# Kernel tuning notes

Hardware: AMD Instinct MI355X
Metric: run time of the kernel (lower is better)

The kernel has to match this reference:

```python
import jax, jax.numpy as jnp
import numpy as np

N_NODES = 50000
N_EDGES = 800000
D_IN = 128
D_H = 128
N_LAYERS = 3
N_CLASSES = 10
NUM_GRAPHS = 256
BN_EPS = 1e-5


def _bn(h, gamma, beta):
    # BatchNorm1d, training-mode statistics (biased variance) over node axis
    mu = jnp.mean(h, axis=0)
    var = jnp.mean((h - mu) ** 2, axis=0)
    return (h - mu) * jax.lax.rsqrt(var + BN_EPS) * gamma + beta


def setup_inputs() -> dict:
    key = jax.random.key(0)
    ks = jax.random.split(key, 16)
    x = jax.random.normal(ks[0], (N_NODES, D_IN), dtype=jnp.float32)
    edge_index = jax.random.randint(ks[1], (2, N_EDGES), 0, N_NODES, dtype=jnp.int64)
    batch = jnp.sort(jax.random.randint(ks[2], (N_NODES,), 0, NUM_GRAPHS, dtype=jnp.int64))
    s1 = 1.0 / np.sqrt(D_IN)
    s2 = 1.0 / np.sqrt(D_H)
    W1 = jax.random.uniform(ks[3], (N_LAYERS, D_IN, D_H), jnp.float32, -s1, s1)
    b1 = jax.random.uniform(ks[4], (N_LAYERS, D_H), jnp.float32, -s1, s1)
    g1 = jnp.ones((N_LAYERS, D_H), jnp.float32)
    bt1 = jnp.zeros((N_LAYERS, D_H), jnp.float32)
    W2 = jax.random.uniform(ks[5], (N_LAYERS, D_H, D_H), jnp.float32, -s2, s2)
    b2 = jax.random.uniform(ks[6], (N_LAYERS, D_H), jnp.float32, -s2, s2)
    g2 = jnp.ones((N_LAYERS, D_H), jnp.float32)
    bt2 = jnp.zeros((N_LAYERS, D_H), jnp.float32)
    sc = 1.0 / np.sqrt(D_H * N_LAYERS)
    Wc1 = jax.random.uniform(ks[7], (D_H * N_LAYERS, D_H), jnp.float32, -sc, sc)
    bc1 = jax.random.uniform(ks[8], (D_H,), jnp.float32, -sc, sc)
    Wc2 = jax.random.uniform(ks[9], (D_H, N_CLASSES), jnp.float32, -s2, s2)
    bc2 = jax.random.uniform(ks[10], (N_CLASSES,), jnp.float32, -s2, s2)
    return {"x": x, "edge_index": edge_index, "batch": batch,
            "W1": W1, "b1": b1, "g1": g1, "bt1": bt1,
            "W2": W2, "b2": b2, "g2": g2, "bt2": bt2,
            "Wc1": Wc1, "bc1": bc1, "Wc2": Wc2, "bc2": bc2}


def reference(x, edge_index, batch, W1, b1, g1, bt1, W2, b2, g2, bt2, Wc1, bc1, Wc2, bc2):
    src = edge_index[0]
    dst = edge_index[1]
    readouts = []
    h = x
    for i in range(N_LAYERS):
        # GINConv, eps=0: (1+eps)*h + sum_{j->i} h_j, then MLP
        agg = jax.ops.segment_sum(h[src], dst, num_segments=N_NODES)  # [N, d]
        z = h + agg
        z = z @ W1[i] + b1[i]
        z = jax.nn.relu(_bn(z, g1[i], bt1[i]))
        z = z @ W2[i] + b2[i]
        # outer BN + ReLU
        h = jax.nn.relu(_bn(z, g2[i], bt2[i]))
        readouts.append(jax.ops.segment_sum(h, batch, num_segments=NUM_GRAPHS))
    h_graph = jnp.concatenate(readouts, axis=1)  # [G, L*d]
    # classifier (dropout in eval mode -> identity)
    out = jax.nn.relu(h_graph @ Wc1 + bc1) @ Wc2 + bc2
    return out
```

## Files before the change

### kernel.cpp

```cpp
#include <hip/hip_runtime.h>

#define N_NODES 50000
#define N_EDGES 800000
#define D 128
#define NLAYERS 3
#define N_CLASSES 10
#define NUM_GRAPHS 256
#define BN_EPS 1e-5f

#define CHUNKS 64
#define CHSIZE 12500
#define RANGES 4
#define RSIZE 12500
#define SBANKS 8

typedef __attribute__((ext_vector_type(4))) float f4;
typedef __attribute__((ext_vector_type(2))) float f2;
typedef __attribute__((ext_vector_type(4))) int i4;
typedef __attribute__((ext_vector_type(8))) short short8;
typedef __attribute__((ext_vector_type(4))) unsigned short us4;
typedef __attribute__((ext_vector_type(8))) unsigned short us8;

__device__ inline float b2f(unsigned short u) {
    unsigned int i = ((unsigned int)u) << 16;
    return __builtin_bit_cast(float, i);
}
__device__ inline unsigned short f2b(float f) {
    unsigned int u = __builtin_bit_cast(unsigned int, f);
    unsigned int r = (u + 0x7FFFu + ((u >> 16) & 1u)) >> 16;
    return (unsigned short)r;
}

__device__ inline void coef_to_lds(const float* __restrict__ stats,
                                   const float* __restrict__ g,
                                   const float* __restrict__ bt,
                                   float* ac_sm, int tid) {
    if (tid < D) {
        float s = 0.f, q = 0.f;
#pragma unroll
        for (int b = 0; b < SBANKS; b++) {
            s += stats[b * 2 * D + tid];
            q += stats[b * 2 * D + D + tid];
        }
        float mu = s * (1.0f / N_NODES);
        float var = q * (1.0f / N_NODES) - mu * mu;
        float inv = rsqrtf(var + BN_EPS);
        float a = g[tid] * inv;
        ac_sm[tid] = a;
        ac_sm[D + tid] = bt[tid] - mu * a;
    }
}


__global__ __launch_bounds__(256) void k_ph(const int* __restrict__ dst,
                                            int* __restrict__ pos,
                                            int* __restrict__ ph) {
    __shared__ int h[RSIZE];
    int c = blockIdx.x, r = blockIdx.y;
    int t = threadIdx.x;
    for (int i = t; i < RSIZE; i += 256) h[i] = 0;
    __syncthreads();
    int base = c * CHSIZE;
    int lo = r * RSIZE;
    const i4* dst4 = (const i4*)(dst + base);
    for (int j = t; j < CHSIZE / 4; j += 256) {
        i4 dv = dst4[j];
#pragma unroll
        for (int u = 0; u < 4; u++) {
            int d = dv[u] - lo;
            if ((unsigned)d < RSIZE) pos[base + j * 4 + u] = atomicAdd(&h[d], 1);
        }
    }
    __syncthreads();
    int* outp = ph + (size_t)c * N_NODES + lo;
    for (int i = t; i < RSIZE; i += 256) outp[i] = h[i];
}

__global__ __launch_bounds__(256) void k_m1(int* __restrict__ ph,
                                            const int* __restrict__ bat,
                                            int* __restrict__ deg,
                                            int* __restrict__ bsum,
                                            int* __restrict__ gp) {
    __shared__ int sm[256];
    int t = threadIdx.x;
    int b = blockIdx.x * 256 + t;
    int s = 0;
    if (b < N_NODES) {
#pragma unroll 4
        for (int c = 0; c < CHUNKS; c++) {
            int v = ph[(size_t)c * N_NODES + b];
            ph[(size_t)c * N_NODES + b] = s;
            s += v;
        }
        deg[b] = s;
    }
    sm[t] = s;
    __syncthreads();
    for (int off = 128; off > 0; off >>= 1) {
        if (t < off) sm[t] += sm[t + off];
        __syncthreads();
    }
    if (t == 0) bsum[blockIdx.x] = sm[0];
    if (b < N_NODES) {
        int bb = bat[b];
        int prev = (b == 0) ? -1 : bat[b - 1];
        for (int g = prev + 1; g <= bb; g++) gp[g] = b;
        if (b == N_NODES - 1)
            for (int g = bb + 1; g <= NUM_GRAPHS; g++) gp[g] = N_NODES;
    }
}


__global__ __launch_bounds__(256) void k_xw(const float* __restrict__ x,
                                            const float* __restrict__ W1,
                                            const float* __restrict__ W2,
                                            us4* __restrict__ xb,
                                            short8* __restrict__ Wb) {
    int gid = blockIdx.x * 256 + threadIdx.x;
    const f4* xf = (const f4*)x;
#pragma unroll
    for (int rep = 0; rep < 2; rep++) {
        int i = gid + rep * 800000;
        f4 v = xf[i];
        us4 o;
        o[0] = f2b(v.x); o[1] = f2b(v.y); o[2] = f2b(v.z); o[3] = f2b(v.w);
        xb[i] = o;
    }
    if (gid < 6 * 32 * 64) {
        int m = gid >> 11;
        int f = (gid >> 6) & 31;
        int l = gid & 63;
        int ct = f >> 2, ks = f & 3;
        int n = ct * 16 + (l & 15);
        int k0 = ks * 32 + (l >> 4) * 8;
        const float* Wsrc = (m < 3) ? (W1 + (size_t)m * D * D) : (W2 + (size_t)(m - 3) * D * D);
        short8 o;
#pragma unroll
        for (int j = 0; j < 8; j++) o[j] = (short)f2b(Wsrc[(size_t)(k0 + j) * D + n]);
        Wb[gid] = o;
    }
}


__global__ void k_s2(int* __restrict__ bsum, int* __restrict__ rowp) {
    __shared__ int sm[256];
    int t = threadIdx.x;
    int v = (t < 196) ? bsum[t] : 0;
    sm[t] = v;
    __syncthreads();
    for (int off = 1; off < 256; off <<= 1) {
        int u = (t >= off) ? sm[t - off] : 0;
        __syncthreads();
        sm[t] += u;
        __syncthreads();
    }
    if (t < 196) bsum[t] = sm[t] - v;
    if (t == 195) rowp[N_NODES] = sm[t];
}

__global__ void k_s3(const int* __restrict__ deg, const int* __restrict__ bsum,
                     int* __restrict__ rowp) {
    __shared__ int sm[256];
    int t = threadIdx.x;
    int i = blockIdx.x * 256 + t;
    int v = (i < N_NODES) ? deg[i] : 0;
    sm[t] = v;
    __syncthreads();
    for (int off = 1; off < 256; off <<= 1) {
        int u = (t >= off) ? sm[t - off] : 0;
        __syncthreads();
        sm[t] += u;
        __syncthreads();
    }
    if (i < N_NODES) rowp[i] = bsum[blockIdx.x] + sm[t] - v;
}

__global__ __launch_bounds__(256) void k_scatter(const int* __restrict__ src,
                                                 const int* __restrict__ dst,
                                                 const int* __restrict__ pos,
                                                 const int* __restrict__ ph,
                                                 const int* __restrict__ rowp,
                                                 int* __restrict__ csr) {
    int e0 = (blockIdx.x * 256 + threadIdx.x) * 4;
    if (e0 >= N_EDGES) return;
    i4 sv = *(const i4*)(src + e0);
    i4 dv = *(const i4*)(dst + e0);
    i4 pv = *(const i4*)(pos + e0);
#pragma unroll
    for (int u = 0; u < 4; u++) {
        int cc = (e0 + u) / CHSIZE;
        int d = dv[u];
        csr[rowp[d] + ph[(size_t)cc * N_NODES + d] + pv[u]] = sv[u];
    }
}


template <bool APPLY_T>
__global__ __launch_bounds__(256) void k_agg(const us8* __restrict__ H,
                                             const float* __restrict__ stats,
                                             const float* __restrict__ g,
                                             const float* __restrict__ bt,
                                             const int* __restrict__ rowp,
                                             const int* __restrict__ csr,
                                             us8* __restrict__ U) {
    __shared__ float ac_sm[2 * D];
    int tid = threadIdx.x;
    if (APPLY_T) {
        coef_to_lds(stats, g, bt, ac_sm, tid);
        __syncthreads();
    }
    int gid = blockIdx.x * 256 + tid;
    int node = gid >> 4;
    int lane = tid & 15;
    float av[8], cv[8];
    if (APPLY_T) {
#pragma unroll
        for (int i = 0; i < 8; i++) {
            av[i] = ac_sm[lane * 8 + i];
            cv[i] = ac_sm[D + lane * 8 + i];
        }
    }
    float s[8] = {0.f, 0.f, 0.f, 0.f, 0.f, 0.f, 0.f, 0.f};
    auto accum = [&](us8 v) {
#pragma unroll
        for (int i = 0; i < 8; i++) {
            float f = b2f(v[i]);
            if (APPLY_T) f = fmaxf(f * av[i] + cv[i], 0.f);
            s[i] += f;
        }
    };
    accum(H[(size_t)node * 16 + lane]);
    int beg = rowp[node], end = rowp[node + 1];
    int j = beg;
    for (; j + 8 <= end; j += 8) {
        int idx[8];
#pragma unroll
        for (int u = 0; u < 8; u++) idx[u] = csr[j + u];
        us8 v[8];
#pragma unroll
        for (int u = 0; u < 8; u++) v[u] = H[(size_t)idx[u] * 16 + lane];
#pragma unroll
        for (int u = 0; u < 8; u++) accum(v[u]);
    }
    for (; j + 2 <= end; j += 2) {
        int i0 = csr[j], i1 = csr[j + 1];
        us8 v0 = H[(size_t)i0 * 16 + lane];
        us8 v1 = H[(size_t)i1 * 16 + lane];
        accum(v0); accum(v1);
    }
    if (j < end) accum(H[(size_t)csr[j] * 16 + lane]);
    us8 o;
#pragma unroll
    for (int i = 0; i < 8; i++) o[i] = f2b(s[i]);
    U[(size_t)node * 16 + lane] = o;
}


template <bool TRANS>
__global__ __launch_bounds__(256) void k_gemm(const unsigned short* __restrict__ A,
                                              const short8* __restrict__ Wb,
                                              const float* __restrict__ bias,
                                              const float* __restrict__ stats_in,
                                              const float* __restrict__ g,
                                              const float* __restrict__ bt,
                                              unsigned short* __restrict__ Z,
                                              float* __restrict__ stats_out, int M) {
    __shared__ float lds_s[D], lds_q[D];
    __shared__ float ac_sm[2 * D];
    int tid = threadIdx.x;
    if (tid < D) { lds_s[tid] = 0.f; lds_q[tid] = 0.f; }
    if (TRANS) coef_to_lds(stats_in, g, bt, ac_sm, tid);
    int w = tid >> 6, l = tid & 63;
    int lr = l & 15, lg = l >> 4;
    int rowb0 = blockIdx.x * 128 + w * 32;
    f4 acc[2][8];
#pragma unroll
    for (int ct = 0; ct < 8; ct++) {
        float bv = bias[ct * 16 + lr];
#pragma unroll
        for (int rt = 0; rt < 2; rt++) {
            acc[rt][ct].x = bv; acc[rt][ct].y = bv; acc[rt][ct].z = bv; acc[rt][ct].w = bv;
        }
    }
    __syncthreads();

#pragma unroll
    for (int ks = 0; ks < 4; ks++) {
        short8 a[2];
#pragma unroll
        for (int rt = 0; rt < 2; rt++) {
            int arow = rowb0 + rt * 16 + lr;
            int arow_c = arow < M ? arow : M - 1;
            if (!TRANS) {
                a[rt] = *(const short8*)(A + (size_t)arow_c * D + ks * 32 + lg * 8);
            } else {
                int k0 = ks * 32 + lg * 8;
                const unsigned short* ap = A + (size_t)arow_c * D + k0;
                us4 v0 = *(const us4*)ap;
                us4 v1 = *(const us4*)(ap + 4);
                f4 a0 = *(const f4*)&ac_sm[k0];
                f4 a1 = *(const f4*)&ac_sm[k0 + 4];
                f4 c0 = *(const f4*)&ac_sm[D + k0];
                f4 c1 = *(const f4*)&ac_sm[D + k0 + 4];
                a[rt][0] = (short)f2b(fmaxf(b2f(v0[0]) * a0.x + c0.x, 0.f));
                a[rt][1] = (short)f2b(fmaxf(b2f(v0[1]) * a0.y + c0.y, 0.f));
                a[rt][2] = (short)f2b(fmaxf(b2f(v0[2]) * a0.z + c0.z, 0.f));
                a[rt][3] = (short)f2b(fmaxf(b2f(v0[3]) * a0.w + c0.w, 0.f));
                a[rt][4] = (short)f2b(fmaxf(b2f(v1[0]) * a1.x + c1.x, 0.f));
                a[rt][5] = (short)f2b(fmaxf(b2f(v1[1]) * a1.y + c1.y, 0.f));
                a[rt][6] = (short)f2b(fmaxf(b2f(v1[2]) * a1.z + c1.z, 0.f));
                a[rt][7] = (short)f2b(fmaxf(b2f(v1[3]) * a1.w + c1.w, 0.f));
            }
        }
#pragma unroll
        for (int ct = 0; ct < 8; ct++) {
            short8 b = Wb[(ct * 4 + ks) * 64 + l];
            acc[0][ct] = __builtin_amdgcn_mfma_f32_16x16x32_bf16(a[0], b, acc[0][ct], 0, 0, 0);
            acc[1][ct] = __builtin_amdgcn_mfma_f32_16x16x32_bf16(a[1], b, acc[1][ct], 0, 0, 0);
        }
    }

#pragma unroll
    for (int ct = 0; ct < 8; ct++) {
        float s = 0.f, q = 0.f;
#pragma unroll
        for (int rt = 0; rt < 2; rt++) {
#pragma unroll
            for (int r = 0; r < 4; r++) {
                float v = acc[rt][ct][r];
                int rd = rowb0 + rt * 16 + lg * 4 + r;
                float m = rd < M ? 1.f : 0.f;
                s += v * m;
                q += v * v * m;
                if (rd < M) Z[(size_t)rd * D + ct * 16 + lr] = f2b(v);
            }
        }
        s += __shfl_xor(s, 16);
        s += __shfl_xor(s, 32);
        q += __shfl_xor(q, 16);
        q += __shfl_xor(q, 32);
        if (lg == 0) {
            atomicAdd(&lds_s[ct * 16 + lr], s);
            atomicAdd(&lds_q[ct * 16 + lr], q);
        }
    }
    __syncthreads();
    int bank = blockIdx.x & (SBANKS - 1);
    if (tid < D) {
        atomicAdd(&stats_out[bank * 2 * D + tid], lds_s[tid]);
        atomicAdd(&stats_out[bank * 2 * D + D + tid], lds_q[tid]);
    }
}


__global__ __launch_bounds__(256) void k_readout(const unsigned int* __restrict__ Zb,
                                                 const float* __restrict__ stats,
                                                 const float* __restrict__ g,
                                                 const float* __restrict__ bt,
                                                 const int* __restrict__ gp,
                                                 const int* __restrict__ batch,
                                                 float* __restrict__ ro, int layer) {
    __shared__ f2 sm[256];
    __shared__ float ac_sm[2 * D];
    int tid = threadIdx.x;
    coef_to_lds(stats, g, bt, ac_sm, tid);
    __syncthreads();
    int n0 = blockIdx.x * 256;
    int n1 = n0 + 256; if (n1 > N_NODES) n1 = N_NODES;
    int g_lo = batch[n0], g_hi = batch[n1 - 1];
    int grp = tid >> 6, cw = tid & 63;
    float a0 = ac_sm[2 * cw], a1 = ac_sm[2 * cw + 1];
    float c0 = ac_sm[D + 2 * cw], c1 = ac_sm[D + 2 * cw + 1];
    for (int gg = g_lo; gg <= g_hi; gg++) {
        int beg = gp[gg]; if (beg < n0) beg = n0;
        int end = gp[gg + 1]; if (end > n1) end = n1;
        f2 acc; acc.x = 0.f; acc.y = 0.f;
        for (int r = beg + grp; r < end; r += 4) {
            unsigned int v = Zb[(size_t)r * 64 + cw];
            float x0 = b2f((unsigned short)(v & 0xFFFFu));
            float x1 = b2f((unsigned short)(v >> 16));
            acc.x += fmaxf(x0 * a0 + c0, 0.f);
            acc.y += fmaxf(x1 * a1 + c1, 0.f);
        }
        sm[tid] = acc;
        __syncthreads();
        if (tid < 64) {
            f2 t = sm[tid];
            t.x += sm[tid + 64].x + sm[tid + 128].x + sm[tid + 192].x;
            t.y += sm[tid + 64].y + sm[tid + 128].y + sm[tid + 192].y;
            atomicAdd(&ro[(size_t)gg * (NLAYERS * D) + layer * D + 2 * cw], t.x);
            atomicAdd(&ro[(size_t)gg * (NLAYERS * D) + layer * D + 2 * cw + 1], t.y);
        }
        __syncthreads();
    }
}


__global__ void k_cls(const float* __restrict__ ro, const float* __restrict__ Wc1,
                      const float* __restrict__ bc1, const float* __restrict__ Wc2,
                      const float* __restrict__ bc2, float* __restrict__ out) {
    __shared__ float r_sm[NLAYERS * D];
    __shared__ float h_sm[D];
    int g = blockIdx.x;
    int t = threadIdx.x;
    for (int i = t; i < NLAYERS * D; i += D) r_sm[i] = ro[(size_t)g * (NLAYERS * D) + i];
    __syncthreads();
    float acc = bc1[t];
    for (int k = 0; k < NLAYERS * D; k++) acc += r_sm[k] * Wc1[(size_t)k * D + t];
    h_sm[t] = fmaxf(acc, 0.f);
    __syncthreads();
    if (t < N_CLASSES) {
        float o = bc2[t];
        for (int k = 0; k < D; k++) o += h_sm[k] * Wc2[k * N_CLASSES + t];
        out[g * N_CLASSES + t] = o;
    }
}


extern "C" void kernel_launch(void* const* d_in, const int* in_sizes, int n_in,
                              void* d_out, int out_size, void* d_ws, size_t ws_size,
                              hipStream_t stream) {
    const float* x   = (const float*)d_in[0];
    const int*   ei  = (const int*)d_in[1];
    const int*   bat = (const int*)d_in[2];
    const float* W1  = (const float*)d_in[3];
    const float* b1  = (const float*)d_in[4];
    const float* g1  = (const float*)d_in[5];
    const float* bt1 = (const float*)d_in[6];
    const float* W2  = (const float*)d_in[7];
    const float* b2  = (const float*)d_in[8];
    const float* g2  = (const float*)d_in[9];
    const float* bt2 = (const float*)d_in[10];
    const float* Wc1 = (const float*)d_in[11];
    const float* bc1 = (const float*)d_in[12];
    const float* Wc2 = (const float*)d_in[13];
    const float* bc2 = (const float*)d_in[14];
    float* out = (float*)d_out;

    const int* src = ei;
    const int* dst = ei + N_EDGES;

    char* ws = (char*)d_ws;
    size_t off = 0;
    auto alloc = [&](size_t bytes) -> void* {
        void* p = ws + off;
        off += (bytes + 255) & ~(size_t)255;
        return p;
    };
    float* stats = (float*)alloc(6 * SBANKS * 2 * D * sizeof(float));
    float* ro    = (float*)alloc((size_t)NUM_GRAPHS * NLAYERS * D * sizeof(float));
    size_t zero_bytes = off;
    int*   deg   = (int*)alloc(N_NODES * sizeof(int));
    int*   gp    = (int*)alloc((NUM_GRAPHS + 1) * sizeof(int));
    int*   bsum  = (int*)alloc(256 * sizeof(int));
    int*   rowp  = (int*)alloc((N_NODES + 1) * sizeof(int));
    int*   pos   = (int*)alloc(N_EDGES * sizeof(int));
    int*   csr   = (int*)alloc(N_EDGES * sizeof(int));
    const size_t NBH = (size_t)N_NODES * D * sizeof(unsigned short);
    unsigned short* xb   = (unsigned short*)alloc(NBH);
    unsigned short* bufA = (unsigned short*)alloc(NBH);
    unsigned short* bufB = (unsigned short*)alloc(NBH);
    unsigned short* bufC = (unsigned short*)alloc(NBH);
    short8* Wb   = (short8*)alloc(6 * 32 * 64 * sizeof(short8));
    int* ph = (int*)bufB;

    hipMemsetAsync(ws, 0, zero_bytes, stream);

    k_ph<<<dim3(CHUNKS, RANGES), 256, 0, stream>>>(dst, pos, ph);
    k_m1<<<196, 256, 0, stream>>>(ph, bat, deg, bsum, gp);
    k_xw<<<3125, 256, 0, stream>>>(x, W1, W2, (us4*)xb, Wb);
    k_s2<<<1, 256, 0, stream>>>(bsum, rowp);
    k_s3<<<196, 256, 0, stream>>>(deg, bsum, rowp);
    k_scatter<<<(N_EDGES / 4 + 255) / 256, 256, 0, stream>>>(src, dst, pos, ph, rowp, csr);

    const int gemm_grid = (N_NODES + 127) / 128;
    const unsigned short* H = xb;
    for (int i = 0; i < NLAYERS; i++) {
        float* st1 = stats + (size_t)(2 * i) * SBANKS * 2 * D;
        float* st2 = stats + (size_t)(2 * i + 1) * SBANKS * 2 * D;
        float* st2p = stats + (size_t)(2 * i - 1) * SBANKS * 2 * D;
        if (i == 0)
            k_agg<false><<<3125, 256, 0, stream>>>((const us8*)H, nullptr, nullptr, nullptr,
                                                   rowp, csr, (us8*)bufA);
        else
            k_agg<true><<<3125, 256, 0, stream>>>((const us8*)H, st2p, g2 + (i - 1) * D,
                                                  bt2 + (i - 1) * D, rowp, csr, (us8*)bufA);
        k_gemm<false><<<gemm_grid, 256, 0, stream>>>(bufA, Wb + (size_t)i * 2048, b1 + i * D,
                                                     nullptr, nullptr, nullptr, bufB, st1, N_NODES);
        k_gemm<true><<<gemm_grid, 256, 0, stream>>>(bufB, Wb + (size_t)(3 + i) * 2048, b2 + i * D,
                                                    st1, g1 + i * D, bt1 + i * D, bufC, st2, N_NODES);
        k_readout<<<196, 256, 0, stream>>>((const unsigned int*)bufC, st2, g2 + i * D, bt2 + i * D,
                                           gp, bat, ro, i);
        H = bufC;
    }
    k_cls<<<NUM_GRAPHS, 128, 0, stream>>>(ro, Wc1, bc1, Wc2, bc2, out);
}
```

Baseline: 346.7 us.

## Slice feature buffers into 16-column planes, sort nodes by degree, use 16-bit indices

Node feature buffers are stored as 8 feature slices of 16 columns each. Each aggregation block now works on one slice, so the gathered working set per pass is smaller and more cache friendly. Nodes are also reordered by degree through a histogram and permutation, so threads within a wave see similar neighbour counts, which cuts divergence. CSR indices and positions become 16-bit to halve index traffic. The 16-bit node ids and positions rely on node ids fitting in unsigned short, but N_NODES is 50000, which fits.

```diff
diff --git a/kernel.cpp b/kernel.cpp
--- a/kernel.cpp
+++ b/kernel.cpp
@@ -13,6 +13,8 @@
 #define RANGES 4
 #define RSIZE 12500
 #define SBANKS 8
+#define NBLK 196
+#define SLICE 800000
 
 typedef __attribute__((ext_vector_type(4))) float f4;
 typedef __attribute__((ext_vector_type(2))) float f2;
@@ -31,6 +33,7 @@
     return (unsigned short)r;
 }
 
+
 __device__ inline void coef_to_lds(const float* __restrict__ stats,
                                    const float* __restrict__ g,
                                    const float* __restrict__ bt,
@@ -53,7 +56,7 @@
 
 
 __global__ __launch_bounds__(256) void k_ph(const int* __restrict__ dst,
-                                            int* __restrict__ pos,
+                                            unsigned short* __restrict__ pos,
                                             int* __restrict__ ph) {
     __shared__ int h[RSIZE];
     int c = blockIdx.x, r = blockIdx.y;
@@ -68,7 +71,7 @@
 #pragma unroll
         for (int u = 0; u < 4; u++) {
             int d = dv[u] - lo;
-            if ((unsigned)d < RSIZE) pos[base + j * 4 + u] = atomicAdd(&h[d], 1);
+            if ((unsigned)d < RSIZE) pos[base + j * 4 + u] = (unsigned short)atomicAdd(&h[d], 1);
         }
     }
     __syncthreads();
@@ -80,9 +83,12 @@
                                             const int* __restrict__ bat,
                                             int* __restrict__ deg,
                                             int* __restrict__ bsum,
-                                            int* __restrict__ gp) {
+                                            int* __restrict__ gp,
+                                            int* __restrict__ bh) {
     __shared__ int sm[256];
+    __shared__ int hist[64];
     int t = threadIdx.x;
+    if (t < 64) hist[t] = 0;
     int b = blockIdx.x * 256 + t;
     int s = 0;
     if (b < N_NODES) {
@@ -96,11 +102,13 @@
     }
     sm[t] = s;
     __syncthreads();
+    if (b < N_NODES) atomicAdd(&hist[min(s, 63)], 1);
     for (int off = 128; off > 0; off >>= 1) {
         if (t < off) sm[t] += sm[t + off];
         __syncthreads();
     }
     if (t == 0) bsum[blockIdx.x] = sm[0];
+    if (t < 64) bh[blockIdx.x * 64 + t] = hist[t];
     if (b < N_NODES) {
         int bb = bat[b];
         int prev = (b == 0) ? -1 : bat[b - 1];
@@ -114,7 +122,7 @@
 __global__ __launch_bounds__(256) void k_xw(const float* __restrict__ x,
                                             const float* __restrict__ W1,
                                             const float* __restrict__ W2,
-                                            us4* __restrict__ xb,
+                                            unsigned short* __restrict__ xb,
                                             short8* __restrict__ Wb) {
     int gid = blockIdx.x * 256 + threadIdx.x;
     const f4* xf = (const f4*)x;
@@ -124,7 +132,9 @@
         f4 v = xf[i];
         us4 o;
         o[0] = f2b(v.x); o[1] = f2b(v.y); o[2] = f2b(v.z); o[3] = f2b(v.w);
-        xb[i] = o;
+        int n = i >> 5;
+        int f0 = (i & 31) * 4;
+        *(us4*)(xb + (size_t)(f0 >> 4) * SLICE + (size_t)n * 16 + (f0 & 15)) = o;
     }
     if (gid < 6 * 32 * 64) {
         int m = gid >> 11;
@@ -142,10 +152,10 @@
 }
 
 
-__global__ void k_s2(int* __restrict__ bsum, int* __restrict__ rowp) {
+__global__ void k_s2(int* __restrict__ bsum, int* __restrict__ rowp, int* __restrict__ bh) {
     __shared__ int sm[256];
     int t = threadIdx.x;
-    int v = (t < 196) ? bsum[t] : 0;
+    int v = (t < NBLK) ? bsum[t] : 0;
     sm[t] = v;
     __syncthreads();
     for (int off = 1; off < 256; off <<= 1) {
@@ -154,14 +164,39 @@
         sm[t] += u;
         __syncthreads();
     }
-    if (t < 196) bsum[t] = sm[t] - v;
-    if (t == 195) rowp[N_NODES] = sm[t];
-}
+    if (t < NBLK) bsum[t] = sm[t] - v;
+    if (t == NBLK - 1) rowp[N_NODES] = sm[t];
+    __syncthreads();
+    int tot = 0;
+    if (t < 64) {
+        for (int blk = 0; blk < NBLK; blk++) tot += bh[blk * 64 + t];
+    }
+    sm[t] = (t < 64) ? tot : 0;
+    __syncthreads();
+    for (int off = 1; off < 64; off <<= 1) {
+        int u = (t >= off && t < 64) ? sm[t - off] : 0;
+        __syncthreads();
+        if (t < 64) sm[t] += u;
+        __syncthreads();
+    }
+    if (t < 64) {
+        int run = sm[t] - tot;
+        for (int blk = 0; blk < NBLK; blk++) {
+            int tmp = bh[blk * 64 + t];
+            bh[blk * 64 + t] = run;
+            run += tmp;
+        }
+    }
+}
+
 
 __global__ void k_s3(const int* __restrict__ deg, const int* __restrict__ bsum,
-                     int* __restrict__ rowp) {
+                     int* __restrict__ rowp, const int* __restrict__ bh,
+                     unsigned short* __restrict__ perm) {
     __shared__ int sm[256];
+    __shared__ int lh[64];
     int t = threadIdx.x;
+    if (t < 64) lh[t] = 0;
     int i = blockIdx.x * 256 + t;
     int v = (i < N_NODES) ? deg[i] : 0;
     sm[t] = v;
@@ -172,64 +207,76 @@
         sm[t] += u;
         __syncthreads();
     }
-    if (i < N_NODES) rowp[i] = bsum[blockIdx.x] + sm[t] - v;
+    if (i < N_NODES) {
+        rowp[i] = bsum[blockIdx.x] + sm[t] - v;
+        int bk = min(v, 63);
+        int p = atomicAdd(&lh[bk], 1);
+        perm[bh[blockIdx.x * 64 + bk] + p] = (unsigned short)i;
+    }
 }
 
 __global__ __launch_bounds__(256) void k_scatter(const int* __restrict__ src,
                                                  const int* __restrict__ dst,
-                                                 const int* __restrict__ pos,
+                                                 const unsigned short* __restrict__ pos,
                                                  const int* __restrict__ ph,
                                                  const int* __restrict__ rowp,
-                                                 int* __restrict__ csr) {
+                                                 unsigned short* __restrict__ csr) {
     int e0 = (blockIdx.x * 256 + threadIdx.x) * 4;
     if (e0 >= N_EDGES) return;
     i4 sv = *(const i4*)(src + e0);
     i4 dv = *(const i4*)(dst + e0);
-    i4 pv = *(const i4*)(pos + e0);
+    us4 pv = *(const us4*)(pos + e0);
 #pragma unroll
     for (int u = 0; u < 4; u++) {
         int cc = (e0 + u) / CHSIZE;
         int d = dv[u];
-        csr[rowp[d] + ph[(size_t)cc * N_NODES + d] + pv[u]] = sv[u];
+        csr[rowp[d] + ph[(size_t)cc * N_NODES + d] + (int)pv[u]] = (unsigned short)sv[u];
     }
 }
 
 
 template <bool APPLY_T>
-__global__ __launch_bounds__(256) void k_agg(const us8* __restrict__ H,
+__global__ __launch_bounds__(256) void k_agg(const unsigned short* __restrict__ H,
                                              const float* __restrict__ stats,
                                              const float* __restrict__ g,
                                              const float* __restrict__ bt,
                                              const int* __restrict__ rowp,
-                                             const int* __restrict__ csr,
-                                             us8* __restrict__ U) {
+                                             const unsigned short* __restrict__ csr,
+                                             const unsigned short* __restrict__ perm,
+                                             unsigned short* __restrict__ U) {
     __shared__ float ac_sm[2 * D];
     int tid = threadIdx.x;
     if (APPLY_T) {
         coef_to_lds(stats, g, bt, ac_sm, tid);
         __syncthreads();
     }
-    int gid = blockIdx.x * 256 + tid;
-    int node = gid >> 4;
-    int lane = tid & 15;
+    int s = blockIdx.x & 7;
+    int chunk = blockIdx.x >> 3;
+    int li = chunk * 128 + (tid >> 1);
+    if (li >= N_NODES) return;
+    int node = perm[li];
+    int lane = tid & 1;
+    const unsigned short* Hs = H + (size_t)s * SLICE;
+    unsigned short* Us = U + (size_t)s * SLICE;
     float av[8], cv[8];
     if (APPLY_T) {
+        int f0 = s * 16 + lane * 8;
 #pragma unroll
         for (int i = 0; i < 8; i++) {
-            av[i] = ac_sm[lane * 8 + i];
-            cv[i] = ac_sm[D + lane * 8 + i];
-        }
-    }
-    float s[8] = {0.f, 0.f, 0.f, 0.f, 0.f, 0.f, 0.f, 0.f};
+            av[i] = ac_sm[f0 + i];
+            cv[i] = ac_sm[D + f0 + i];
+        }
+    }
+    float acc[8] = {0.f, 0.f, 0.f, 0.f, 0.f, 0.f, 0.f, 0.f};
     auto accum = [&](us8 v) {
 #pragma unroll
         for (int i = 0; i < 8; i++) {
             float f = b2f(v[i]);
             if (APPLY_T) f = fmaxf(f * av[i] + cv[i], 0.f);
-            s[i] += f;
+            acc[i] += f;
         }
     };
-    accum(H[(size_t)node * 16 + lane]);
+    accum(*(const us8*)(Hs + (size_t)node * 16 + lane * 8));
     int beg = rowp[node], end = rowp[node + 1];
     int j = beg;
     for (; j + 8 <= end; j += 8) {
@@ -238,21 +285,15 @@
         for (int u = 0; u < 8; u++) idx[u] = csr[j + u];
         us8 v[8];
 #pragma unroll
-        for (int u = 0; u < 8; u++) v[u] = H[(size_t)idx[u] * 16 + lane];
+        for (int u = 0; u < 8; u++) v[u] = *(const us8*)(Hs + (size_t)idx[u] * 16 + lane * 8);
 #pragma unroll
         for (int u = 0; u < 8; u++) accum(v[u]);
     }
-    for (; j + 2 <= end; j += 2) {
-        int i0 = csr[j], i1 = csr[j + 1];
-        us8 v0 = H[(size_t)i0 * 16 + lane];
-        us8 v1 = H[(size_t)i1 * 16 + lane];
-        accum(v0); accum(v1);
-    }
-    if (j < end) accum(H[(size_t)csr[j] * 16 + lane]);
+    for (; j < end; j++) accum(*(const us8*)(Hs + (size_t)csr[j] * 16 + lane * 8));
     us8 o;
 #pragma unroll
-    for (int i = 0; i < 8; i++) o[i] = f2b(s[i]);
-    U[(size_t)node * 16 + lane] = o;
+    for (int i = 0; i < 8; i++) o[i] = f2b(acc[i]);
+    *(us8*)(Us + (size_t)node * 16 + lane * 8) = o;
 }
 
 
@@ -287,15 +328,16 @@
 #pragma unroll
     for (int ks = 0; ks < 4; ks++) {
         short8 a[2];
+        int k0 = ks * 32 + lg * 8;
+        const unsigned short* As = A + (size_t)(k0 >> 4) * SLICE + (k0 & 15);
 #pragma unroll
         for (int rt = 0; rt < 2; rt++) {
             int arow = rowb0 + rt * 16 + lr;
             int arow_c = arow < M ? arow : M - 1;
+            const unsigned short* ap = As + (size_t)arow_c * 16;
             if (!TRANS) {
-                a[rt] = *(const short8*)(A + (size_t)arow_c * D + ks * 32 + lg * 8);
+                a[rt] = *(const short8*)ap;
             } else {
-                int k0 = ks * 32 + lg * 8;
-                const unsigned short* ap = A + (size_t)arow_c * D + k0;
                 us4 v0 = *(const us4*)ap;
                 us4 v1 = *(const us4*)(ap + 4);
                 f4 a0 = *(const f4*)&ac_sm[k0];
@@ -323,6 +365,7 @@
 #pragma unroll
     for (int ct = 0; ct < 8; ct++) {
         float s = 0.f, q = 0.f;
+        unsigned short* Zs = Z + (size_t)ct * SLICE + lr;
 #pragma unroll
         for (int rt = 0; rt < 2; rt++) {
 #pragma unroll
@@ -332,7 +375,7 @@
                 float m = rd < M ? 1.f : 0.f;
                 s += v * m;
                 q += v * v * m;
-                if (rd < M) Z[(size_t)rd * D + ct * 16 + lr] = f2b(v);
+                if (rd < M) Zs[(size_t)rd * 16] = f2b(v);
             }
         }
         s += __shfl_xor(s, 16);
@@ -353,7 +396,7 @@
 }
 
 
-__global__ __launch_bounds__(256) void k_readout(const unsigned int* __restrict__ Zb,
+__global__ __launch_bounds__(256) void k_readout(const unsigned short* __restrict__ Zb,
                                                  const float* __restrict__ stats,
                                                  const float* __restrict__ g,
                                                  const float* __restrict__ bt,
@@ -369,6 +412,7 @@
     int n1 = n0 + 256; if (n1 > N_NODES) n1 = N_NODES;
     int g_lo = batch[n0], g_hi = batch[n1 - 1];
     int grp = tid >> 6, cw = tid & 63;
+    const unsigned short* Zs = Zb + (size_t)(cw >> 3) * SLICE + ((2 * cw) & 15);
     float a0 = ac_sm[2 * cw], a1 = ac_sm[2 * cw + 1];
     float c0 = ac_sm[D + 2 * cw], c1 = ac_sm[D + 2 * cw + 1];
     for (int gg = g_lo; gg <= g_hi; gg++) {
@@ -376,7 +420,7 @@
         int end = gp[gg + 1]; if (end > n1) end = n1;
         f2 acc; acc.x = 0.f; acc.y = 0.f;
         for (int r = beg + grp; r < end; r += 4) {
-            unsigned int v = Zb[(size_t)r * 64 + cw];
+            unsigned int v = *(const unsigned int*)(Zs + (size_t)r * 16);
             float x0 = b2f((unsigned short)(v & 0xFFFFu));
             float x1 = b2f((unsigned short)(v >> 16));
             acc.x += fmaxf(x0 * a0 + c0, 0.f);
@@ -454,8 +498,10 @@
     int*   gp    = (int*)alloc((NUM_GRAPHS + 1) * sizeof(int));
     int*   bsum  = (int*)alloc(256 * sizeof(int));
     int*   rowp  = (int*)alloc((N_NODES + 1) * sizeof(int));
-    int*   pos   = (int*)alloc(N_EDGES * sizeof(int));
-    int*   csr   = (int*)alloc(N_EDGES * sizeof(int));
+    int*   bh    = (int*)alloc(NBLK * 64 * sizeof(int));
+    unsigned short* pos  = (unsigned short*)alloc(N_EDGES * sizeof(unsigned short));
+    unsigned short* csr  = (unsigned short*)alloc(N_EDGES * sizeof(unsigned short));
+    unsigned short* perm = (unsigned short*)alloc(N_NODES * sizeof(unsigned short));
     const size_t NBH = (size_t)N_NODES * D * sizeof(unsigned short);
     unsigned short* xb   = (unsigned short*)alloc(NBH);
     unsigned short* bufA = (unsigned short*)alloc(NBH);
@@ -467,12 +513,13 @@
     hipMemsetAsync(ws, 0, zero_bytes, stream);
 
     k_ph<<<dim3(CHUNKS, RANGES), 256, 0, stream>>>(dst, pos, ph);
-    k_m1<<<196, 256, 0, stream>>>(ph, bat, deg, bsum, gp);
-    k_xw<<<3125, 256, 0, stream>>>(x, W1, W2, (us4*)xb, Wb);
-    k_s2<<<1, 256, 0, stream>>>(bsum, rowp);
-    k_s3<<<196, 256, 0, stream>>>(deg, bsum, rowp);
+    k_m1<<<NBLK, 256, 0, stream>>>(ph, bat, deg, bsum, gp, bh);
+    k_xw<<<3125, 256, 0, stream>>>(x, W1, W2, xb, Wb);
+    k_s2<<<1, 256, 0, stream>>>(bsum, rowp, bh);
+    k_s3<<<NBLK, 256, 0, stream>>>(deg, bsum, rowp, bh, perm);
     k_scatter<<<(N_EDGES / 4 + 255) / 256, 256, 0, stream>>>(src, dst, pos, ph, rowp, csr);
 
+    const int agg_grid  = 8 * ((N_NODES + 127) / 128);
     const int gemm_grid = (N_NODES + 127) / 128;
     const unsigned short* H = xb;
     for (int i = 0; i < NLAYERS; i++) {
@@ -480,17 +527,17 @@
         float* st2 = stats + (size_t)(2 * i + 1) * SBANKS * 2 * D;
         float* st2p = stats + (size_t)(2 * i - 1) * SBANKS * 2 * D;
         if (i == 0)
-            k_agg<false><<<3125, 256, 0, stream>>>((const us8*)H, nullptr, nullptr, nullptr,
-                                                   rowp, csr, (us8*)bufA);
+            k_agg<false><<<agg_grid, 256, 0, stream>>>(H, nullptr, nullptr, nullptr,
+                                                       rowp, csr, perm, bufA);
         else
-            k_agg<true><<<3125, 256, 0, stream>>>((const us8*)H, st2p, g2 + (i - 1) * D,
-                                                  bt2 + (i - 1) * D, rowp, csr, (us8*)bufA);
+            k_agg<true><<<agg_grid, 256, 0, stream>>>(H, st2p, g2 + (i - 1) * D,
+                                                      bt2 + (i - 1) * D, rowp, csr, perm, bufA);
         k_gemm<false><<<gemm_grid, 256, 0, stream>>>(bufA, Wb + (size_t)i * 2048, b1 + i * D,
                                                      nullptr, nullptr, nullptr, bufB, st1, N_NODES);
         k_gemm<true><<<gemm_grid, 256, 0, stream>>>(bufB, Wb + (size_t)(3 + i) * 2048, b2 + i * D,
                                                     st1, g1 + i * D, bt1 + i * D, bufC, st2, N_NODES);
-        k_readout<<<196, 256, 0, stream>>>((const unsigned int*)bufC, st2, g2 + i * D, bt2 + i * D,
-                                           gp, bat, ro, i);
+        k_readout<<<NBLK, 256, 0, stream>>>(bufC, st2, g2 + i * D, bt2 + i * D,
+                                            gp, bat, ro, i);
         H = bufC;
     }
     k_cls<<<NUM_GRAPHS, 128, 0, stream>>>(ro, Wc1, bc1, Wc2, bc2, out);
```

After: 371.7 us. 1.07x slower.
